# Kernel tuning notes

Measured on AMD Instinct MI355X. Metric: run time of the kernel, lower is better.

Reference implementation:

```python
import jax, jax.numpy as jnp
import numpy as np

D = 1024

def setup_inputs() -> dict:
    key = jax.random.key(0)
    ks = jax.random.split(key, 7)
    s = 1.0 / np.sqrt(D)  # torch Linear default init scale (uniform bound)
    x = jax.random.normal(ks[0], (4, 2048, D), dtype=jnp.float32)
    Wq = jax.random.uniform(ks[1], (D, D), jnp.float32, -s, s)
    Wk = jax.random.uniform(ks[2], (D, D), jnp.float32, -s, s)
    Wv = jax.random.uniform(ks[3], (D, D), jnp.float32, -s, s)
    bq = jax.random.uniform(ks[4], (D,), jnp.float32, -s, s)
    bk = jax.random.uniform(ks[5], (D,), jnp.float32, -s, s)
    bv = jax.random.uniform(ks[6], (D,), jnp.float32, -s, s)
    return {"x": x, "Wq": Wq, "bq": bq, "Wk": Wk, "bk": bk, "Wv": Wv, "bv": bv}

def reference(x, Wq, bq, Wk, bk, Wv, bv):
    # Linear layers: y = x @ W^T + b (weights stored torch-style [out, in])
    Q = jnp.einsum('bsd,ed->bse', x, Wq) + bq
    K = jnp.einsum('bsd,ed->bse', x, Wk) + bk
    V = jnp.einsum('bsd,ed->bse', x, Wv) + bv
    scale = jnp.sqrt(jnp.asarray(Q.shape[-1], Q.dtype))
    scores = jnp.einsum('bqd,bkd->bqk', Q, K) / scale  # [B, S, S]
    probs = jax.nn.softmax(scores, axis=-1)
    return jnp.einsum('bqk,bkd->bqd', probs, V)
```

## Files before the change

### kernel.cpp

```cpp
#include <hip/hip_runtime.h>


typedef __bf16 bf16x8 __attribute__((ext_vector_type(8)));
typedef float f32x4 __attribute__((ext_vector_type(4)));
typedef unsigned short u16;

__device__ __forceinline__ u16 f2b(float f) {
  union { float f; unsigned u; } a; a.f = f;
  unsigned r = a.u + 0x7fffu + ((a.u >> 16) & 1u);
  return (u16)(r >> 16);
}

__device__ __forceinline__ int xcd_swz(int p) {
  return (p & 7) * 32 + (p >> 3);
}

__global__ __launch_bounds__(256) void cast_all_kernel(const float* __restrict__ x,
                                                       const float* __restrict__ Wq,
                                                       const float* __restrict__ Wk,
                                                       const float* __restrict__ Wv,
                                                       u16* __restrict__ xb,
                                                       u16* __restrict__ Wb) {
  int b = blockIdx.x;
  if (b < 8192) {
    const int i = b * 256 + threadIdx.x;
    float4 v = reinterpret_cast<const float4*>(x)[i];
    reinterpret_cast<ushort4*>(xb)[i] =
        make_ushort4(f2b(v.x), f2b(v.y), f2b(v.z), f2b(v.w));
  } else {
    b -= 8192;
    const int w = b >> 10;
    const float* src = (w == 0) ? Wq : (w == 1) ? Wk : Wv;
    const int i = (b & 1023) * 256 + threadIdx.x;
    float4 v = reinterpret_cast<const float4*>(src)[i];
    reinterpret_cast<ushort4*>(Wb + (size_t)w * 1048576)[i] =
        make_ushort4(f2b(v.x), f2b(v.y), f2b(v.z), f2b(v.w));
  }
}

template <int GEOM, int NT>
__device__ __forceinline__ void core2(const char* __restrict__ Ab,
                                      const char* __restrict__ Bb, int lda, int ldb,
                                      char* smem, f32x4* acc) {
  constexpr int LDSBUF = GEOM ? 49152 : 65536;
  constexpr int BOFF = GEOM ? 16384 : 32768;
  constexpr int AHALF = GEOM ? 8192 : 16384;
  constexpr int NA = GEOM ? 4 : 8;
  const int tid = threadIdx.x;
  const int wave = tid >> 6, lane = tid & 63;
  const int wr = wave >> 2, wc = wave & 3;
  const int fr = lane & 15, fg = lane >> 4;
  const int rd = (fr * 64 + fg * 16) ^ (((fr >> 3) & 1) << 5);
  const int li = (lane * 16) ^ ((lane >> 5) << 5);
  const int sr = li >> 6, sc2 = li & 63;

  auto STAGE = [&](int kt, int s) {
    char* base = smem + (kt & 1) * LDSBUF;
    const int colOff = kt * 128 + s * 64 + sc2;
    char* ldsA = base + s * AHALF;
    __builtin_amdgcn_global_load_lds(
        (const __attribute__((address_space(1))) void*)(Ab + (size_t)(wave * 16 + sr) * lda + colOff),
        (__attribute__((address_space(3))) void*)(ldsA + wave * 1024), 16, 0, 0);
    if constexpr (GEOM == 0)
      __builtin_amdgcn_global_load_lds(
          (const __attribute__((address_space(1))) void*)(Ab + (size_t)((8 + wave) * 16 + sr) * lda + colOff),
          (__attribute__((address_space(3))) void*)(ldsA + 8192 + wave * 1024), 16, 0, 0);
    char* ldsB = base + BOFF + s * 16384;
    __builtin_amdgcn_global_load_lds(
        (const __attribute__((address_space(1))) void*)(Bb + (size_t)(wave * 16 + sr) * ldb + colOff),
        (__attribute__((address_space(3))) void*)(ldsB + wave * 1024), 16, 0, 0);
    __builtin_amdgcn_global_load_lds(
        (const __attribute__((address_space(1))) void*)(Bb + (size_t)((8 + wave) * 16 + sr) * ldb + colOff),
        (__attribute__((address_space(3))) void*)(ldsB + 8192 + wave * 1024), 16, 0, 0);
  };

  STAGE(0, 0);
  STAGE(0, 1);
  if constexpr (GEOM == 0) asm volatile("s_waitcnt vmcnt(4)" ::: "memory");
  else asm volatile("s_waitcnt vmcnt(3)" ::: "memory");
  __builtin_amdgcn_s_barrier();
  __builtin_amdgcn_sched_barrier(0);

  for (int kt = 0; kt < NT; ++kt) {
    const char* bufA = smem + (kt & 1) * LDSBUF;
    const char* bufB = bufA + BOFF;
#pragma unroll
    for (int s = 0; s < 2; ++s) {
      bf16x8 afr[NA], bfr[4];
#pragma unroll
      for (int m = 0; m < NA; ++m)
        afr[m] = *reinterpret_cast<const bf16x8*>(bufA + s * AHALF + (wr * NA + m) * 1024 + rd);
#pragma unroll
      for (int n = 0; n < 4; ++n)
        bfr[n] = *reinterpret_cast<const bf16x8*>(bufB + s * 16384 + (wc * 4 + n) * 1024 + rd);
      if (kt + 1 < NT) STAGE(kt + 1, s);
      __builtin_amdgcn_s_barrier();
      __builtin_amdgcn_sched_barrier(0);
      __builtin_amdgcn_s_setprio(1);
#pragma unroll
      for (int m = 0; m < NA; ++m)
#pragma unroll
        for (int n = 0; n < 4; ++n)
          acc[m * 4 + n] = __builtin_amdgcn_mfma_f32_16x16x32_bf16(
              afr[m], bfr[n], acc[m * 4 + n], 0, 0, 0);
      __builtin_amdgcn_s_setprio(0);
      if (kt < NT - 1) {
        if constexpr (GEOM == 0) asm volatile("s_waitcnt vmcnt(4)" ::: "memory");
        else asm volatile("s_waitcnt vmcnt(3)" ::: "memory");
      } else if (s == 0) {
        asm volatile("s_waitcnt vmcnt(0)" ::: "memory");
      }
      __builtin_amdgcn_s_barrier();
      __builtin_amdgcn_sched_barrier(0);
    }
  }
}

__global__ __launch_bounds__(512, 2) void qkproj_kernel(
    const u16* __restrict__ A, const u16* __restrict__ Bm,
    const float* __restrict__ bq, const float* __restrict__ bk,
    u16* __restrict__ QK) {
  extern __shared__ char smem[];
  const int wk = xcd_swz(blockIdx.x);
  const int bx = wk & 31, by = wk >> 5;
  const int tileM = bx * 256, tileN = by * 256;
  f32x4 acc[32] = {};
  core2<0, 16>((const char*)A + (size_t)tileM * 2048,
               (const char*)Bm + (size_t)tileN * 2048, 2048, 2048, smem, acc);
  const int tid = threadIdx.x;
  const int wave = tid >> 6, lane = tid & 63;
  const int wr = wave >> 2, wc = wave & 3, fr = lane & 15, fg = lane >> 4;
  const int w = by >> 2;
  const float* bias = (w == 0) ? bq : bk;
  u16* O = QK + (size_t)w * 8388608;
#pragma unroll
  for (int mi = 0; mi < 8; ++mi) {
    const int r0 = tileM + wr * 128 + mi * 16 + fg * 4;
#pragma unroll
    for (int n = 0; n < 4; ++n) {
      const int cw = (tileN + wc * 64 + n * 16 + fr) & 1023;
      const float bi = bias[cw];
#pragma unroll
      for (int jj = 0; jj < 4; ++jj)
        O[(size_t)(r0 + jj) * 1024 + cw] = f2b(acc[mi * 4 + n][jj] + bi);
    }
  }
}

__global__ __launch_bounds__(512, 2) void vproj_kernel(
    const u16* __restrict__ A, const u16* __restrict__ Bv,
    const float* __restrict__ bvv, u16* __restrict__ Vt) {
  extern __shared__ char smem[];
  const int wk = xcd_swz(blockIdx.x);
  const int bx = wk & 63, by = wk >> 6;
  const int tileM = bx * 128, tileN = by * 256;
  f32x4 acc[16] = {};
  core2<1, 16>((const char*)A + (size_t)tileM * 2048,
               (const char*)Bv + (size_t)tileN * 2048, 2048, 2048, smem, acc);
  const int tid = threadIdx.x;
  const int wave = tid >> 6, lane = tid & 63;
  const int wr = wave >> 2, wc = wave & 3, fr = lane & 15, fg = lane >> 4;
#pragma unroll
  for (int mi = 0; mi < 4; ++mi) {
    const int r0 = tileM + wr * 64 + mi * 16 + fg * 4;
    const int b = r0 >> 11, s0 = r0 & 2047;
#pragma unroll
    for (int n = 0; n < 4; ++n) {
      const int cw = (tileN + wc * 64 + n * 16 + fr) & 1023;
      const float bi = bvv[cw];
      ushort4 u = make_ushort4(f2b(acc[mi * 4 + n][0] + bi), f2b(acc[mi * 4 + n][1] + bi),
                               f2b(acc[mi * 4 + n][2] + bi), f2b(acc[mi * 4 + n][3] + bi));
      *reinterpret_cast<ushort4*>(&Vt[(size_t)b * 2097152 + (size_t)cw * 2048 + s0]) = u;
    }
  }
}

__global__ __launch_bounds__(512, 2) void sc8_kernel(const u16* __restrict__ Qb,
                                                     const u16* __restrict__ Kb,
                                                     u16* __restrict__ P,
                                                     float* __restrict__ rowpart) {
  extern __shared__ char smem[];
  const int wk = xcd_swz(blockIdx.x);
  const int bx = wk & 7, by = (wk >> 3) & 7, z = wk >> 6;
  const int tileM = bx * 256, tileN = by * 256;
  f32x4 acc[32] = {};
  core2<0, 16>((const char*)Qb + (size_t)z * 4194304 + (size_t)tileM * 2048,
               (const char*)Kb + (size_t)z * 4194304 + (size_t)tileN * 2048, 2048, 2048,
               smem, acc);
  const int tid = threadIdx.x;
  const int wave = tid >> 6, lane = tid & 63;
  const int wr = wave >> 2, wc = wave & 3, fr = lane & 15, fg = lane >> 4;
  float* rs = (float*)smem;
  u16* Po = P + (size_t)z * 4194304 + (size_t)tileM * 2048 + tileN;
#pragma unroll
  for (int mi = 0; mi < 8; ++mi) {
#pragma unroll
    for (int jj = 0; jj < 4; ++jj) {
      const int rl = wr * 128 + mi * 16 + fg * 4 + jj;
      float part = 0.f;
#pragma unroll
      for (int n = 0; n < 4; ++n) {
        float e = __expf(acc[mi * 4 + n][jj] * 0.03125f);
        part += e;
        Po[(size_t)rl * 2048 + wc * 64 + n * 16 + fr] = f2b(e);
      }
      part += __shfl_xor(part, 1);
      part += __shfl_xor(part, 2);
      part += __shfl_xor(part, 4);
      part += __shfl_xor(part, 8);
      if (fr == 0) rs[wc * 256 + rl] = part;
    }
  }
  __syncthreads();
  if (tid < 256) {
    float s = rs[tid] + rs[256 + tid] + rs[512 + tid] + rs[768 + tid];
    rowpart[(size_t)by * 8192 + z * 2048 + tileM + tid] = s;
  }
}

__global__ __launch_bounds__(512, 2) void pv8_kernel(const u16* __restrict__ P,
                                                     const u16* __restrict__ Vt,
                                                     const float* __restrict__ rowpart,
                                                     float* __restrict__ out) {
  extern __shared__ char smem[];
  const int wk = xcd_swz(blockIdx.x);
  const int bx = wk & 15, by = (wk >> 4) & 3, z = wk >> 6;
  const int tileM = bx * 128, tileN = by * 256;
  float* rinv = (float*)(smem + 98304);
  const int tid = threadIdx.x;
  if (tid < 128) {
    float s = 0.f;
#pragma unroll
    for (int t = 0; t < 8; ++t) s += rowpart[t * 8192 + z * 2048 + tileM + tid];
    rinv[tid] = 1.0f / s;
  }
  __builtin_amdgcn_sched_barrier(0);
  f32x4 acc[16] = {};
  core2<1, 32>((const char*)P + (size_t)z * 8388608 + (size_t)tileM * 4096,
               (const char*)Vt + (size_t)z * 4194304 + (size_t)tileN * 4096, 4096, 4096,
               smem, acc);
  const int wave = tid >> 6, lane = tid & 63;
  const int wr = wave >> 2, wc = wave & 3, fr = lane & 15, fg = lane >> 4;
  float* O = out + (size_t)z * 2097152;
#pragma unroll
  for (int mi = 0; mi < 4; ++mi) {
#pragma unroll
    for (int jj = 0; jj < 4; ++jj) {
      const int r = wr * 64 + mi * 16 + fg * 4 + jj;
      const float inv = rinv[r];
#pragma unroll
      for (int n = 0; n < 4; ++n)
        O[(size_t)(tileM + r) * 1024 + tileN + wc * 64 + n * 16 + fr] =
            acc[mi * 4 + n][jj] * inv;
    }
  }
}

extern "C" void kernel_launch(void* const* d_in, const int* in_sizes, int n_in,
                              void* d_out, int out_size, void* d_ws, size_t ws_size,
                              hipStream_t stream) {
  if (ws_size < ((size_t)72 << 20)) return;
  const float* x = (const float*)d_in[0];
  const float* Wq = (const float*)d_in[1];
  const float* bq = (const float*)d_in[2];
  const float* Wk = (const float*)d_in[3];
  const float* bk = (const float*)d_in[4];
  const float* Wv = (const float*)d_in[5];
  const float* bv = (const float*)d_in[6];
  char* ws = (char*)d_ws;
  u16* xb = (u16*)(ws);
  u16* Pb = (u16*)(ws);
  u16* Qb = (u16*)(ws + ((size_t)16 << 20));
  u16* Kb = (u16*)(ws + ((size_t)32 << 20));
  u16* Vt = (u16*)(ws + ((size_t)48 << 20));
  u16* Wb = (u16*)(ws + ((size_t)64 << 20));
  float* rowpart = (float*)(ws + ((size_t)70 << 20));
  float* out = (float*)d_out;

  (void)hipFuncSetAttribute((const void*)qkproj_kernel,
                            hipFuncAttributeMaxDynamicSharedMemorySize, 131072);
  (void)hipFuncSetAttribute((const void*)vproj_kernel,
                            hipFuncAttributeMaxDynamicSharedMemorySize, 98304);
  (void)hipFuncSetAttribute((const void*)sc8_kernel,
                            hipFuncAttributeMaxDynamicSharedMemorySize, 131072);
  (void)hipFuncSetAttribute((const void*)pv8_kernel,
                            hipFuncAttributeMaxDynamicSharedMemorySize, 98816);

  cast_all_kernel<<<11264, 256, 0, stream>>>(x, Wq, Wk, Wv, xb, Wb);

  qkproj_kernel<<<256, 512, 131072, stream>>>(xb, Wb, bq, bk, Qb);
  vproj_kernel<<<256, 512, 98304, stream>>>(xb, Wb + 2097152, bv, Vt);

  sc8_kernel<<<256, 512, 131072, stream>>>(Qb, Kb, Pb, rowpart);
  pv8_kernel<<<256, 512, 98816, stream>>>(Pb, Vt, rowpart, out);
}
```

Before: 156.9 us.

## Split 256x256 GEMM mainloop into finer-grained staged phases with deeper prefetch

```diff
diff --git a/kernel.cpp b/kernel.cpp
--- a/kernel.cpp
+++ b/kernel.cpp
@@ -38,14 +38,10 @@
   }
 }
 
-template <int GEOM, int NT>
-__device__ __forceinline__ void core2(const char* __restrict__ Ab,
-                                      const char* __restrict__ Bb, int lda, int ldb,
-                                      char* smem, f32x4* acc) {
-  constexpr int LDSBUF = GEOM ? 49152 : 65536;
-  constexpr int BOFF = GEOM ? 16384 : 32768;
-  constexpr int AHALF = GEOM ? 8192 : 16384;
-  constexpr int NA = GEOM ? 4 : 8;
+template <int NT>
+__device__ __forceinline__ void core8g0(const char* __restrict__ Ab,
+                                        const char* __restrict__ Bb, int lda, int ldb,
+                                        char* smem, f32x4* acc) {
   const int tid = threadIdx.x;
   const int wave = tid >> 6, lane = tid & 63;
   const int wr = wave >> 2, wc = wave & 3;
@@ -54,18 +50,89 @@
   const int li = (lane * 16) ^ ((lane >> 5) << 5);
   const int sr = li >> 6, sc2 = li & 63;
 
+  auto STAGE = [&](int kt, int p) {
+    const int isB = p & 1, s = p >> 1;
+    char* lds = smem + (kt & 1) * 65536 + (isB ? 32768 + s * 16384 : s * 16384);
+    const char* gb = isB ? Bb : Ab;
+    const int ldx = isB ? ldb : lda;
+    const int colOff = kt * 128 + s * 64 + sc2;
+    __builtin_amdgcn_global_load_lds(
+        (const __attribute__((address_space(1))) void*)(gb + (size_t)(wave * 16 + sr) * ldx + colOff),
+        (__attribute__((address_space(3))) void*)(lds + wave * 1024), 16, 0, 0);
+    __builtin_amdgcn_global_load_lds(
+        (const __attribute__((address_space(1))) void*)(gb + (size_t)((8 + wave) * 16 + sr) * ldx + colOff),
+        (__attribute__((address_space(3))) void*)(lds + 8192 + wave * 1024), 16, 0, 0);
+  };
+
+#pragma unroll
+  for (int p = 0; p < 4; ++p) STAGE(0, p);
+  STAGE(1, 0);
+  STAGE(1, 1);
+  asm volatile("s_waitcnt vmcnt(8)" ::: "memory");
+  __builtin_amdgcn_s_barrier();
+  __builtin_amdgcn_sched_barrier(0);
+
+  bf16x8 bfr[4];
+  for (int kt = 0; kt < NT; ++kt) {
+    const char* bufA = smem + (kt & 1) * 65536;
+    const char* bufB = bufA + 32768;
+#pragma unroll
+    for (int p = 0; p < 4; ++p) {
+      const int s = p >> 1, j = p & 1;
+      bf16x8 afr[4];
+      if (j == 0) {
+#pragma unroll
+        for (int n = 0; n < 4; ++n)
+          bfr[n] = *reinterpret_cast<const bf16x8*>(bufB + s * 16384 + (wc * 4 + n) * 1024 + rd);
+      }
+#pragma unroll
+      for (int m = 0; m < 4; ++m)
+        afr[m] = *reinterpret_cast<const bf16x8*>(bufA + s * 16384 + (wr * 8 + j * 4 + m) * 1024 + rd);
+      if (p < 2) { if (kt + 1 < NT) STAGE(kt + 1, p + 2); }
+      else       { if (kt + 2 < NT) STAGE(kt + 2, p - 2); }
+      __builtin_amdgcn_s_barrier();
+      __builtin_amdgcn_sched_barrier(0);
+      __builtin_amdgcn_s_setprio(1);
+#pragma unroll
+      for (int m = 0; m < 4; ++m)
+#pragma unroll
+        for (int n = 0; n < 4; ++n)
+          acc[(j * 4 + m) * 4 + n] = __builtin_amdgcn_mfma_f32_16x16x32_bf16(
+              afr[m], bfr[n], acc[(j * 4 + m) * 4 + n], 0, 0, 0);
+      __builtin_amdgcn_s_setprio(0);
+      if (p == 1) {
+        if (kt < NT - 1) asm volatile("s_waitcnt vmcnt(8)" ::: "memory");
+        else asm volatile("s_waitcnt vmcnt(0)" ::: "memory");
+      } else if (p == 3) {
+        if (kt < NT - 2) asm volatile("s_waitcnt vmcnt(8)" ::: "memory");
+        else if (kt == NT - 2) asm volatile("s_waitcnt vmcnt(4)" ::: "memory");
+      }
+      __builtin_amdgcn_s_barrier();
+      __builtin_amdgcn_sched_barrier(0);
+    }
+  }
+}
+
+template <int NT>
+__device__ __forceinline__ void core2g1(const char* __restrict__ Ab,
+                                        const char* __restrict__ Bb, int lda, int ldb,
+                                        char* smem, f32x4* acc) {
+  const int tid = threadIdx.x;
+  const int wave = tid >> 6, lane = tid & 63;
+  const int wr = wave >> 2, wc = wave & 3;
+  const int fr = lane & 15, fg = lane >> 4;
+  const int rd = (fr * 64 + fg * 16) ^ (((fr >> 3) & 1) << 5);
+  const int li = (lane * 16) ^ ((lane >> 5) << 5);
+  const int sr = li >> 6, sc2 = li & 63;
+
   auto STAGE = [&](int kt, int s) {
-    char* base = smem + (kt & 1) * LDSBUF;
+    char* base = smem + (kt & 1) * 49152;
     const int colOff = kt * 128 + s * 64 + sc2;
-    char* ldsA = base + s * AHALF;
+    char* ldsA = base + s * 8192;
     __builtin_amdgcn_global_load_lds(
         (const __attribute__((address_space(1))) void*)(Ab + (size_t)(wave * 16 + sr) * lda + colOff),
         (__attribute__((address_space(3))) void*)(ldsA + wave * 1024), 16, 0, 0);
-    if constexpr (GEOM == 0)
-      __builtin_amdgcn_global_load_lds(
-          (const __attribute__((address_space(1))) void*)(Ab + (size_t)((8 + wave) * 16 + sr) * lda + colOff),
-          (__attribute__((address_space(3))) void*)(ldsA + 8192 + wave * 1024), 16, 0, 0);
-    char* ldsB = base + BOFF + s * 16384;
+    char* ldsB = base + 16384 + s * 16384;
     __builtin_amdgcn_global_load_lds(
         (const __attribute__((address_space(1))) void*)(Bb + (size_t)(wave * 16 + sr) * ldb + colOff),
         (__attribute__((address_space(3))) void*)(ldsB + wave * 1024), 16, 0, 0);
@@ -76,20 +143,19 @@
 
   STAGE(0, 0);
   STAGE(0, 1);
-  if constexpr (GEOM == 0) asm volatile("s_waitcnt vmcnt(4)" ::: "memory");
-  else asm volatile("s_waitcnt vmcnt(3)" ::: "memory");
+  asm volatile("s_waitcnt vmcnt(3)" ::: "memory");
   __builtin_amdgcn_s_barrier();
   __builtin_amdgcn_sched_barrier(0);
 
   for (int kt = 0; kt < NT; ++kt) {
-    const char* bufA = smem + (kt & 1) * LDSBUF;
-    const char* bufB = bufA + BOFF;
+    const char* bufA = smem + (kt & 1) * 49152;
+    const char* bufB = bufA + 16384;
 #pragma unroll
     for (int s = 0; s < 2; ++s) {
-      bf16x8 afr[NA], bfr[4];
-#pragma unroll
-      for (int m = 0; m < NA; ++m)
-        afr[m] = *reinterpret_cast<const bf16x8*>(bufA + s * AHALF + (wr * NA + m) * 1024 + rd);
+      bf16x8 afr[4], bfr[4];
+#pragma unroll
+      for (int m = 0; m < 4; ++m)
+        afr[m] = *reinterpret_cast<const bf16x8*>(bufA + s * 8192 + (wr * 4 + m) * 1024 + rd);
 #pragma unroll
       for (int n = 0; n < 4; ++n)
         bfr[n] = *reinterpret_cast<const bf16x8*>(bufB + s * 16384 + (wc * 4 + n) * 1024 + rd);
@@ -98,15 +164,14 @@
       __builtin_amdgcn_sched_barrier(0);
       __builtin_amdgcn_s_setprio(1);
 #pragma unroll
-      for (int m = 0; m < NA; ++m)
+      for (int m = 0; m < 4; ++m)
 #pragma unroll
         for (int n = 0; n < 4; ++n)
           acc[m * 4 + n] = __builtin_amdgcn_mfma_f32_16x16x32_bf16(
               afr[m], bfr[n], acc[m * 4 + n], 0, 0, 0);
       __builtin_amdgcn_s_setprio(0);
       if (kt < NT - 1) {
-        if constexpr (GEOM == 0) asm volatile("s_waitcnt vmcnt(4)" ::: "memory");
-        else asm volatile("s_waitcnt vmcnt(3)" ::: "memory");
+        asm volatile("s_waitcnt vmcnt(3)" ::: "memory");
       } else if (s == 0) {
         asm volatile("s_waitcnt vmcnt(0)" ::: "memory");
       }
@@ -125,8 +190,8 @@
   const int bx = wk & 31, by = wk >> 5;
   const int tileM = bx * 256, tileN = by * 256;
   f32x4 acc[32] = {};
-  core2<0, 16>((const char*)A + (size_t)tileM * 2048,
-               (const char*)Bm + (size_t)tileN * 2048, 2048, 2048, smem, acc);
+  core8g0<16>((const char*)A + (size_t)tileM * 2048,
+              (const char*)Bm + (size_t)tileN * 2048, 2048, 2048, smem, acc);
   const int tid = threadIdx.x;
   const int wave = tid >> 6, lane = tid & 63;
   const int wr = wave >> 2, wc = wave & 3, fr = lane & 15, fg = lane >> 4;
@@ -155,8 +220,8 @@
   const int bx = wk & 63, by = wk >> 6;
   const int tileM = bx * 128, tileN = by * 256;
   f32x4 acc[16] = {};
-  core2<1, 16>((const char*)A + (size_t)tileM * 2048,
-               (const char*)Bv + (size_t)tileN * 2048, 2048, 2048, smem, acc);
+  core2g1<16>((const char*)A + (size_t)tileM * 2048,
+              (const char*)Bv + (size_t)tileN * 2048, 2048, 2048, smem, acc);
   const int tid = threadIdx.x;
   const int wave = tid >> 6, lane = tid & 63;
   const int wr = wave >> 2, wc = wave & 3, fr = lane & 15, fg = lane >> 4;
@@ -184,9 +249,9 @@
   const int bx = wk & 7, by = (wk >> 3) & 7, z = wk >> 6;
   const int tileM = bx * 256, tileN = by * 256;
   f32x4 acc[32] = {};
-  core2<0, 16>((const char*)Qb + (size_t)z * 4194304 + (size_t)tileM * 2048,
-               (const char*)Kb + (size_t)z * 4194304 + (size_t)tileN * 2048, 2048, 2048,
-               smem, acc);
+  core8g0<16>((const char*)Qb + (size_t)z * 4194304 + (size_t)tileM * 2048,
+              (const char*)Kb + (size_t)z * 4194304 + (size_t)tileN * 2048, 2048, 2048,
+              smem, acc);
   const int tid = threadIdx.x;
   const int wave = tid >> 6, lane = tid & 63;
   const int wr = wave >> 2, wc = wave & 3, fr = lane & 15, fg = lane >> 4;
@@ -236,9 +301,9 @@
   }
   __builtin_amdgcn_sched_barrier(0);
   f32x4 acc[16] = {};
-  core2<1, 32>((const char*)P + (size_t)z * 8388608 + (size_t)tileM * 4096,
-               (const char*)Vt + (size_t)z * 4194304 + (size_t)tileN * 4096, 4096, 4096,
-               smem, acc);
+  core2g1<32>((const char*)P + (size_t)z * 8388608 + (size_t)tileM * 4096,
+              (const char*)Vt + (size_t)z * 4194304 + (size_t)tileN * 4096, 4096, 4096,
+              smem, acc);
   const int wave = tid >> 6, lane = tid & 63;
   const int wr = wave >> 2, wc = wave & 3, fr = lane & 15, fg = lane >> 4;
   float* O = out + (size_t)z * 2097152;
```

Result: no change. 156.1 us (-0.5%).
